# Optimization experiments

Hardware: AMD Instinct MI355X
Metric: run time of the kernel (lower is better)

Reference implementation:

```python
import jax, jax.numpy as jnp
import numpy as np
from jax import lax

N = 16384
K = 16
EPS = 1e-5


def setup_inputs() -> dict:
    key = jax.random.key(0)
    ks = jax.random.split(key, 10)

    def w(k, shape):
        fan_in = shape[0]
        return jax.random.normal(k, shape, jnp.float32) / np.sqrt(fan_in)

    return {
        "pos": jax.random.normal(ks[0], (N, 3), jnp.float32),
        "normal": jax.random.normal(ks[1], (N, 3), jnp.float32),
        # conv1 mlp: Linear(9,64) -> GroupNorm(8,64) -> ReLU -> Linear(64,64)
        "W1a": w(ks[2], (9, 64)), "b1a": jnp.zeros((64,), jnp.float32),
        "g1": jnp.ones((64,), jnp.float32), "beta1": jnp.zeros((64,), jnp.float32),
        "W1b": w(ks[3], (64, 64)), "b1b": jnp.zeros((64,), jnp.float32),
        # conv2 mlp: Linear(67,64) -> GroupNorm(8,64) -> ReLU -> Linear(64,64)
        "W2a": w(ks[4], (67, 64)), "b2a": jnp.zeros((64,), jnp.float32),
        "g2": jnp.ones((64,), jnp.float32), "beta2": jnp.zeros((64,), jnp.float32),
        "W2b": w(ks[5], (64, 64)), "b2b": jnp.zeros((64,), jnp.float32),
        # conv3 mlp: Linear(67,128) -> GroupNorm(16,128) -> ReLU -> Linear(128,128)
        "W3a": w(ks[6], (67, 128)), "b3a": jnp.zeros((128,), jnp.float32),
        "g3": jnp.ones((128,), jnp.float32), "beta3": jnp.zeros((128,), jnp.float32),
        "W3b": w(ks[7], (128, 128)), "b3b": jnp.zeros((128,), jnp.float32),
    }


def knn_graph(pos, k):
    # [N,N] squared distances; loop=True -> self is included (distance 0).
    sq = jnp.sum(pos * pos, axis=1)
    d2 = sq[:, None] + sq[None, :] - 2.0 * (pos @ pos.T)
    _, nbr = lax.top_k(-d2, k)  # [N,k] neighbor (source) indices per target node
    return nbr


def group_norm(h, gamma, beta, groups):
    # h: [N,k,C]; normalize each group of channels per edge sample.
    n, k, c = h.shape
    hg = h.reshape(n, k, groups, c // groups)
    mu = hg.mean(axis=-1, keepdims=True)
    var = hg.var(axis=-1, keepdims=True)
    hg = (hg - mu) * lax.rsqrt(var + EPS)
    return hg.reshape(n, k, c) * gamma + beta


def pointnet_conv(x, pos, nbr, Wa, ba, gamma, beta, Wb, bb, groups):
    # message: concat(x_j, pos_j - pos_i), MLP per edge, max-aggregate over neighbors
    xj = x[nbr]                              # [N,k,C_in]
    rel = pos[nbr] - pos[:, None, :]         # [N,k,3]
    m = jnp.concatenate([xj, rel], axis=-1)  # [N,k,C_in+3]
    h = m @ Wa + ba
    h = jax.nn.relu(group_norm(h, gamma, beta, groups))
    h = h @ Wb + bb
    return jnp.max(h, axis=1)                # [N,C_out]


def reference(pos, normal, W1a, b1a, g1, beta1, W1b, b1b,
              W2a, b2a, g2, beta2, W2b, b2b,
              W3a, b3a, g3, beta3, W3b, b3b):
    nbr = knn_graph(pos, K)
    h = jnp.concatenate([pos, normal], axis=-1)  # [N,6]
    h1 = jax.nn.relu(pointnet_conv(h, pos, nbr, W1a, b1a, g1, beta1, W1b, b1b, 8))
    h2 = jax.nn.relu(pointnet_conv(h1, pos, nbr, W2a, b2a, g2, beta2, W2b, b2b, 8))
    h3 = jax.nn.relu(pointnet_conv(h2, pos, nbr, W3a, b3a, g3, beta3, W3b, b3b, 16))
    return (h1, h2, h3)
```

## Files before the change

kernel.cpp:

```cpp
#include <hip/hip_runtime.h>
#include <hip/hip_bf16.h>
#include <stdint.h>

typedef unsigned long long u64;
typedef unsigned int u32;
typedef __attribute__((ext_vector_type(8))) short bf16x8;
typedef __attribute__((ext_vector_type(8))) unsigned short u16x8;
typedef __attribute__((ext_vector_type(4))) float f32x4;

__device__ __forceinline__ float ldv(const void* p, size_t idx, int mode) {
  return mode ? __bfloat162float(((const __hip_bfloat16*)p)[idx])
              : ((const float*)p)[idx];
}
__device__ __forceinline__ void stv(void* p, size_t idx, int mode, float v) {
  if (mode) ((__hip_bfloat16*)p)[idx] = __float2bfloat16(v);
  else      ((float*)p)[idx] = v;
}
__device__ __forceinline__ unsigned short f2bfb(float f) {
  u32 u = __float_as_uint(f);
  u32 r = u + 0x7fffu + ((u >> 16) & 1u);
  return (unsigned short)(r >> 16);
}
__device__ __forceinline__ float bfb2f(unsigned short b) {
  return __uint_as_float((u32)b << 16);
}
__device__ __forceinline__ u64 shfl64(u64 v, int src) {
  int lo = __shfl((int)(u32)(v & 0xffffffffu), src, 64);
  int hi = __shfl((int)(u32)(v >> 32), src, 64);
  return ((u64)(u32)hi << 32) | (u32)lo;
}
__device__ __forceinline__ u64 shflxor64(u64 v, int m) {
  int lo = __shfl_xor((int)(u32)(v & 0xffffffffu), m, 64);
  int hi = __shfl_xor((int)(u32)(v >> 32), m, 64);
  return ((u64)(u32)hi << 32) | (u32)lo;
}
__device__ __forceinline__ u64 shfl64w16(u64 v, int src) {
  int lo = __shfl((int)(u32)(v & 0xffffffffu), src, 16);
  int hi = __shfl((int)(u32)(v >> 32), src, 16);
  return ((u64)(u32)hi << 32) | (u32)lo;
}

__device__ __forceinline__ u32 benc(float f) {
  u32 u = __float_as_uint(f);
  return (u & 0x80000000u) ? ~u : (u | 0x80000000u);
}
__device__ __forceinline__ float bdec(u32 k) {
  return (k & 0x80000000u) ? __uint_as_float(k ^ 0x80000000u)
                           : __uint_as_float(~k);
}

__global__ void PointNetSimple_61409442398998_kernel() {}

struct CvtEnt { const void* src; float* dst; int n; };
struct CvtArgs { CvtEnt e[12]; };
struct WEnt { const void* src; unsigned short* dst; int K, N, Kpad; };
struct WArgs { WEnt e[6]; };

__global__ void setup_kernel(const void* __restrict__ pos,
                             const void* __restrict__ nrm,
                             WArgs wa, CvtArgs ca,
                             int* __restrict__ flag,
                             float4* __restrict__ pos4,
                             float* __restrict__ h0, int n) {
  const unsigned short* u16p = (const unsigned short*)pos;
  int cnt = 0;
  for (int k = 0; k < 32; ++k) {
    int e = (u16p[k] >> 7) & 0xff;
    if (e >= 110 && e <= 140) cnt++;
  }
  const int mode = (cnt >= 26) ? 1 : 0;

  const int nprep = n >> 8;
  const int b = blockIdx.x;
  if (b < nprep) {
    int i = b * 256 + threadIdx.x;
    float x = ldv(pos, 3*(size_t)i+0, mode);
    float y = ldv(pos, 3*(size_t)i+1, mode);
    float z = ldv(pos, 3*(size_t)i+2, mode);
    pos4[i] = make_float4(x, y, z, x*x + y*y + z*z);
    h0[6*(size_t)i+0] = x; h0[6*(size_t)i+1] = y; h0[6*(size_t)i+2] = z;
    h0[6*(size_t)i+3] = ldv(nrm, 3*(size_t)i+0, mode);
    h0[6*(size_t)i+4] = ldv(nrm, 3*(size_t)i+1, mode);
    h0[6*(size_t)i+5] = ldv(nrm, 3*(size_t)i+2, mode);
    float bmn[3] = {x, y, z}, bmx[3] = {x, y, z};
#pragma unroll
    for (int m = 32; m; m >>= 1) {
#pragma unroll
      for (int k = 0; k < 3; ++k) {
        bmn[k] = fminf(bmn[k], __shfl_xor(bmn[k], m, 64));
        bmx[k] = fmaxf(bmx[k], __shfl_xor(bmx[k], m, 64));
      }
    }
    if ((threadIdx.x & 63) == 0) {
      u32* bb = (u32*)flag;
#pragma unroll
      for (int k = 0; k < 3; ++k) {
        atomicMin(&bb[4 + k], benc(bmn[k]));
        atomicMax(&bb[7 + k], benc(bmx[k]));
      }
    }
  } else {
    int r = b - nprep;
    if (r < 6) {
      WEnt ent = wa.e[r];
      for (int t = threadIdx.x; t < ent.N * ent.Kpad; t += blockDim.x) {
        int nn = t / ent.Kpad;
        int k  = t - nn * ent.Kpad;
        float v = (k < ent.K) ? ldv(ent.src, (size_t)k * ent.N + nn, mode) : 0.0f;
        ent.dst[t] = f2bfb(v);
      }
      if (r == 0 && threadIdx.x == 0) flag[0] = mode;
    } else {
      for (int t2 = 0; t2 < 12; ++t2) {
        CvtEnt ent = ca.e[t2];
        for (int t = threadIdx.x; t < ent.n; t += blockDim.x)
          ent.dst[t] = ldv(ent.src, t, mode);
      }
    }
  }
}

__device__ __forceinline__ void knn_flush(u64* __restrict__ wbuf, int& cnt,
                                          u64& val, u64& t15, float& th,
                                          int lane) {
  u64 cand = (lane < cnt) ? wbuf[lane] : ~0ull;
#pragma unroll
  for (int k = 2; k <= 64; k <<= 1) {
#pragma unroll
    for (int j = k >> 1; j > 0; j >>= 1) {
      u64 other = shflxor64(cand, j);
      bool up    = ((lane & k) == 0) || (k == 64);
      bool lower = ((lane & j) == 0);
      bool keepMin = (up == lower);
      u64 mn = cand < other ? cand : other;
      u64 mx = cand < other ? other : cand;
      cand = keepMin ? mn : mx;
    }
  }
  u64 rev = shfl64w16(cand, 15 - (lane & 15));
  u64 lo = val < rev ? val : rev;
#pragma unroll
  for (int j = 8; j > 0; j >>= 1) {
    u64 other = shflxor64(lo, j);
    bool lower = ((lane & j) == 0);
    u64 mn = lo < other ? lo : other;
    u64 mx = lo < other ? other : lo;
    lo = lower ? mn : mx;
  }
  val = (lane < 16) ? lo : ~0ull;
  t15 = shfl64(val, 15);
  u32 thb = (u32)(t15 >> 32);
  th = (thb == 0xffffffffu) ? 3.4e38f : __uint_as_float(thb);
  cnt = 0;
}

#define GR 32
#define GR3 (GR*GR*GR)

__global__ __launch_bounds__(256) void hist_kernel(
    const float4* __restrict__ pos4, const u32* __restrict__ bbx,
    int* __restrict__ counts, int* __restrict__ cid, int n) {
  const int i = blockIdx.x * 256 + threadIdx.x;
  if (i >= n) return;
  const float mnx = bdec(bbx[0]), mny = bdec(bbx[1]), mnz = bdec(bbx[2]);
  const float ihx = (float)GR / fmaxf(bdec(bbx[3]) - mnx, 1e-20f);
  const float ihy = (float)GR / fmaxf(bdec(bbx[4]) - mny, 1e-20f);
  const float ihz = (float)GR / fmaxf(bdec(bbx[5]) - mnz, 1e-20f);
  float4 p = pos4[i];
  int cx = min(GR - 1, max(0, (int)((p.x - mnx) * ihx)));
  int cy = min(GR - 1, max(0, (int)((p.y - mny) * ihy)));
  int cz = min(GR - 1, max(0, (int)((p.z - mnz) * ihz)));
  int lin = (cz * GR + cy) * GR + cx;
  cid[i] = lin;
  atomicAdd(&counts[lin], 1);
}

__global__ __launch_bounds__(1024) void scan_kernel(
    const int* __restrict__ counts, int* __restrict__ cellstart,
    int* __restrict__ cursor) {
  __shared__ int part[1024];
  const int t = threadIdx.x;
  const int base = t * 32;
  int v[32];
  int s = 0;
#pragma unroll
  for (int k = 0; k < 32; ++k) { v[k] = counts[base + k]; s += v[k]; }
  part[t] = s;
  __syncthreads();
  for (int d = 1; d < 1024; d <<= 1) {
    int x = (t >= d) ? part[t - d] : 0;
    __syncthreads();
    part[t] += x;
    __syncthreads();
  }
  int off = part[t] - s;
#pragma unroll
  for (int k = 0; k < 32; ++k) {
    cellstart[base + k] = off; cursor[base + k] = off; off += v[k];
  }
  if (t == 1023) { cellstart[GR3] = off; cursor[GR3] = off; }
}

__global__ __launch_bounds__(256) void scatter_kernel(
    const float4* __restrict__ pos4, const int* __restrict__ cid,
    int* __restrict__ cursor, int* __restrict__ sidx,
    float4* __restrict__ spos4, int n) {
  const int i = blockIdx.x * 256 + threadIdx.x;
  if (i >= n) return;
  int dst = atomicAdd(&cursor[cid[i]], 1);
  spos4[dst] = pos4[i];
  sidx[dst]  = i;
}

#define KNN6_WPB 4
__global__ __launch_bounds__(256) void knn6_kernel(
    const float4* __restrict__ spos4,
    const int* __restrict__ sidx, const int* __restrict__ cellstart,
    const u32* __restrict__ bbx, int* __restrict__ nbr, int n) {
  __shared__ u64 buf[KNN6_WPB][72];
  const int tid = threadIdx.x, lane = tid & 63, w = tid >> 6;
  const int g = blockIdx.x * KNN6_WPB + w;
  u64* wbuf = &buf[w][0];
  const float4 pi = spos4[g];
  const int target = sidx[g];

  const float mnx = bdec(bbx[0]), mny = bdec(bbx[1]), mnz = bdec(bbx[2]);
  const float ex = fmaxf(bdec(bbx[3]) - mnx, 1e-20f);
  const float ey = fmaxf(bdec(bbx[4]) - mny, 1e-20f);
  const float ez = fmaxf(bdec(bbx[5]) - mnz, 1e-20f);
  const float ihx = (float)GR / ex, ihy = (float)GR / ey, ihz = (float)GR / ez;
  const float hxf = ex * (1.0f / GR), hyf = ey * (1.0f / GR), hzf = ez * (1.0f / GR);
  const int cx = min(GR - 1, max(0, (int)((pi.x - mnx) * ihx)));
  const int cy = min(GR - 1, max(0, (int)((pi.y - mny) * ihy)));
  const int cz = min(GR - 1, max(0, (int)((pi.z - mnz) * ihz)));

  u64 val = ~0ull, t15 = ~0ull;
  float th = 3.4e38f;
  int cnt = 0, nseen = 0;

  auto procSeg = [&](int p0, int p1) {
    if (p1 <= p0) return;
    nseen += p1 - p0;
#pragma unroll 2
    for (int t0 = p0; t0 < p1; t0 += 64) {
      int gi = t0 + lane;
      bool in = gi < p1;
      float4 a = spos4[in ? gi : (p1 - 1)];
      float d2 = (pi.w + a.w) - 2.0f*(pi.x*a.x + pi.y*a.y + pi.z*a.z);
      d2 = fmaxf(d2, 0.0f);
      bool pass = in && (d2 <= th);
      u64 bal = __ballot(pass);
      if (bal) {
        int pc = __popcll(bal);
        if (cnt + pc > 64) knn_flush(wbuf, cnt, val, t15, th, lane);
        u32 mb = __builtin_amdgcn_mbcnt_lo((u32)bal, 0u);
        mb = __builtin_amdgcn_mbcnt_hi((u32)(bal >> 32), mb);
        if (pass)
          wbuf[cnt + mb] = ((u64)__float_as_uint(d2) << 32) | (u32)sidx[gi];
        cnt += pc;
      }
    }
  };

  const int oc = (cz * GR + cy) * GR + cx;
  const int oLo = cellstart[oc], oHi = cellstart[oc + 1];
  procSeg(oLo, oHi);
  if (cnt > 0) knn_flush(wbuf, cnt, val, t15, th, lane);

  int prevLo = 0, prevHi = -1;
  if (lane == cz) { prevLo = oLo; prevHi = oHi; }

  for (int r = 1; r < GR; ++r) {
    const int z0 = max(cz - r, 0), z1 = min(cz + r, GR - 1);
    const int y0 = max(cy - r, 0), y1 = min(cy + r, GR - 1);
    const int x0 = max(cx - r, 0), x1 = min(cx + r, GR - 1);
    int a0 = 0, a1v = 0, b0 = 0, b1v = 0;
    if (lane >= z0 && lane <= z1) {
      int nLo = cellstart[(lane * GR + y0) * GR + x0];
      int nHi = cellstart[(lane * GR + y1) * GR + x1 + 1];
      if (prevHi < 0) { a0 = nLo; a1v = nHi; }
      else            { a0 = nLo; a1v = prevLo; b0 = prevHi; b1v = nHi; }
      prevLo = nLo; prevHi = nHi;
    }
    for (int z = z0; z <= z1; ++z) {
      int sa0 = __shfl(a0, z, 64), sa1 = __shfl(a1v, z, 64);
      int sb0 = __shfl(b0, z, 64), sb1 = __shfl(b1v, z, 64);
      procSeg(sa0, sa1);
      procSeg(sb0, sb1);
    }
    if (cnt > 0) knn_flush(wbuf, cnt, val, t15, th, lane);
    if (nseen >= n) break;
    float mind = 3.4e38f;
    if (cx - r > 0)      mind = fminf(mind, pi.x - (mnx + (float)(cx - r) * hxf));
    if (cx + r < GR - 1) mind = fminf(mind, (mnx + (float)(cx + r + 1) * hxf) - pi.x);
    if (cy - r > 0)      mind = fminf(mind, pi.y - (mny + (float)(cy - r) * hyf));
    if (cy + r < GR - 1) mind = fminf(mind, (mny + (float)(cy + r + 1) * hyf) - pi.y);
    if (cz - r > 0)      mind = fminf(mind, pi.z - (mnz + (float)(cz - r) * hzf));
    if (cz + r < GR - 1) mind = fminf(mind, (mnz + (float)(cz + r + 1) * hzf) - pi.z);
    float mind2 = mind * mind * 0.9999f - 1e-6f;
    if (mind2 > th) break;
  }
  if (cnt > 0) knn_flush(wbuf, cnt, val, t15, th, lane);
  if (lane < 16) nbr[(size_t)target * 16 + lane] = (int)(val & 0xffffffffu);
}

template<int CIN, int CMID, int KT1, int NT, int KT2>
__global__ __launch_bounds__(256, 4) void conv_mfma6_kernel(
    const float* __restrict__ xf,
    const unsigned short* __restrict__ xb,
    const float4* __restrict__ pos4,
    const int* __restrict__ nbr,
    const int* __restrict__ flag,
    const unsigned short* __restrict__ WaT,
    const unsigned short* __restrict__ WbT,
    const float* __restrict__ baf,
    const float* __restrict__ gmf,
    const float* __restrict__ btf,
    const float* __restrict__ bbf,
    unsigned short* __restrict__ xoutb,
    void* __restrict__ bout, size_t out_off)
{
  constexpr int K1PAD = KT1 * 32;
  constexpr int SB = CMID + 8;

  __shared__ unsigned short msgB[128 * SB];

  const int tid  = threadIdx.x;
  const int lane = tid & 63;
  const int w    = tid >> 6;
  const int quad = lane >> 4;
  const int cl   = lane & 15;
  const int node0 = blockIdx.x * 8;
  const int mode = flag[0];

  bf16x8 afr[2][KT1];
#pragma unroll
  for (int mt = 0; mt < 2; ++mt) {
    const int node = node0 + w*2 + mt;
    const int j = nbr[(size_t)node*16 + cl];
    const float4 pin = pos4[node];
    const float4 pj = pos4[j];
    const float rx = pj.x - pin.x, ry = pj.y - pin.y, rz = pj.z - pin.z;
    if constexpr (CIN == 64) {
#pragma unroll
      for (int kt = 0; kt < 2; ++kt)
        afr[mt][kt] = *(const bf16x8*)&xb[(size_t)j*64 + kt*32 + quad*8];
      unsigned short o[8] = {0,0,0,0,0,0,0,0};
      if (quad == 0) { o[0] = f2bfb(rx); o[1] = f2bfb(ry); o[2] = f2bfb(rz); }
      afr[mt][KT1-1] = *(bf16x8*)o;
    } else {
      unsigned short o[8] = {0,0,0,0,0,0,0,0};
      if (quad == 0) {
        const float* p = &xf[(size_t)j*6];
        o[0] = f2bfb(p[0]); o[1] = f2bfb(p[1]); o[2] = f2bfb(p[2]);
        o[3] = f2bfb(p[3]); o[4] = f2bfb(p[4]); o[5] = f2bfb(p[5]);
        o[6] = f2bfb(rx);   o[7] = f2bfb(ry);
      } else if (quad == 1) {
        o[0] = f2bfb(rz);
      }
      afr[mt][0] = *(bf16x8*)o;
    }
  }

  const int grow = lane >> 1, ggl = lane & 1;
#pragma unroll
  for (int nt = 0; nt < NT; ++nt) {
    f32x4 a1[2];
    a1[0] = (f32x4){0.f, 0.f, 0.f, 0.f};
    a1[1] = (f32x4){0.f, 0.f, 0.f, 0.f};
#pragma unroll
    for (int kt = 0; kt < KT1; ++kt) {
      bf16x8 bfr = *(const bf16x8*)&WaT[(size_t)(nt*16 + cl) * K1PAD + kt*32 + quad*8];
      a1[0] = __builtin_amdgcn_mfma_f32_16x16x32_bf16(afr[0][kt], bfr, a1[0], 0, 0, 0);
      a1[1] = __builtin_amdgcn_mfma_f32_16x16x32_bf16(afr[1][kt], bfr, a1[1], 0, 0, 0);
    }
    float bac = baf[nt*16 + cl];
#pragma unroll
    for (int mt = 0; mt < 2; ++mt)
#pragma unroll
      for (int reg = 0; reg < 4; ++reg)
        msgB[(w*32 + mt*16 + quad*4 + reg) * SB + nt*16 + cl] =
            f2bfb(a1[mt][reg] + bac);
    asm volatile("" ::: "memory");
    {
      const int cb = nt*16 + ggl*8;
      unsigned short* p = &msgB[(w*32 + grow) * SB + cb];
      u16x8 hv = *(const u16x8*)p;
      float vv[8];
#pragma unroll
      for (int e = 0; e < 8; ++e) vv[e] = bfb2f(hv[e]);
      float s = 0.f, q = 0.f;
#pragma unroll
      for (int e = 0; e < 8; ++e) { s += vv[e]; q += vv[e]*vv[e]; }
      float mu = s * 0.125f;
      float var = q * 0.125f - mu * mu;
      float inv = rsqrtf(fmaxf(var, 0.0f) + 1e-5f);
      unsigned short o[8];
#pragma unroll
      for (int e = 0; e < 8; ++e) {
        float t = (vv[e] - mu) * inv * gmf[cb+e] + btf[cb+e];
        o[e] = f2bfb(fmaxf(t, 0.0f));
      }
      *(bf16x8*)p = *(bf16x8*)o;
    }
    asm volatile("" ::: "memory");
  }

  f32x4 acc2[2][NT];
#pragma unroll
  for (int mt = 0; mt < 2; ++mt)
#pragma unroll
    for (int nt = 0; nt < NT; ++nt) acc2[mt][nt] = (f32x4){0.f, 0.f, 0.f, 0.f};
#pragma unroll
  for (int kt = 0; kt < KT2; ++kt) {
    bf16x8 af0 = *(const bf16x8*)&msgB[(w*32 + cl)      * SB + kt*32 + quad*8];
    bf16x8 af1 = *(const bf16x8*)&msgB[(w*32 + 16 + cl) * SB + kt*32 + quad*8];
#pragma unroll
    for (int nt = 0; nt < NT; ++nt) {
      bf16x8 bfr = *(const bf16x8*)&WbT[(size_t)(nt*16 + cl) * CMID + kt*32 + quad*8];
      acc2[0][nt] = __builtin_amdgcn_mfma_f32_16x16x32_bf16(af0, bfr, acc2[0][nt], 0, 0, 0);
      acc2[1][nt] = __builtin_amdgcn_mfma_f32_16x16x32_bf16(af1, bfr, acc2[1][nt], 0, 0, 0);
    }
  }

#pragma unroll
  for (int mt = 0; mt < 2; ++mt) {
    int node = node0 + w*2 + mt;
#pragma unroll
    for (int nt = 0; nt < NT; ++nt) {
      float m = fmaxf(fmaxf(acc2[mt][nt][0], acc2[mt][nt][1]),
                      fmaxf(acc2[mt][nt][2], acc2[mt][nt][3]));
      m = fmaxf(m, __shfl_xor(m, 16, 64));
      m = fmaxf(m, __shfl_xor(m, 32, 64));
      float v = fmaxf(m + bbf[nt*16 + cl], 0.0f);
      if (quad == 0) {
        size_t oi = (size_t)node * CMID + nt*16 + cl;
        if (xoutb) xoutb[oi] = f2bfb(v);
        stv(bout, out_off + oi, mode, v);
      }
    }
  }
}

extern "C" void kernel_launch(void* const* d_in, const int* in_sizes, int n_in,
                              void* d_out, int out_size, void* d_ws, size_t ws_size,
                              hipStream_t stream) {
  (void)n_in; (void)ws_size; (void)in_sizes;
  int n = out_size / 256;
  if (n <= 0 || (n & 255)) n = 16384;

  float* ws = (float*)d_ws;
  int*    flag    = (int*)ws;
  float4* pos4    = (float4*)(ws + 16);
  float*  h0      = ws + 16 + (size_t)4*n;
  int*    nbr     = (int*)(ws + 16 + (size_t)10*n);
  unsigned short* h1b = (unsigned short*)(ws + 16 + (size_t)26*n);
  unsigned short* h2b = (unsigned short*)(ws + 16 + (size_t)58*n);
  float*  vbuf    = ws + 16 + (size_t)90*n;
  unsigned short* wtbuf = (unsigned short*)(vbuf + 1024);

  float* gbase = vbuf + 1024 + 22528;
  int*    cid       = (int*)gbase;
  int*    counts    = cid + n;
  int*    cellstart = counts + GR3;
  int*    cursor    = cellstart + 32772;
  int*    sidx      = cursor + 32772;
  float4* spos4     = (float4*)(sidx + n);

  const int vsz[12] = {64,64,64,64, 64,64,64,64, 128,128,128,128};
  const int vsrc[12] = {3,4,5,7, 9,10,11,13, 15,16,17,19};
  CvtArgs ca;
  float* vptr[12];
  {
    int off = 0;
    for (int t = 0; t < 12; ++t) {
      ca.e[t].src = d_in[vsrc[t]];
      ca.e[t].dst = vbuf + off;
      ca.e[t].n   = vsz[t];
      vptr[t] = vbuf + off;
      off += vsz[t];
    }
  }
  const int wK[6]    = {9, 64, 67, 64, 67, 128};
  const int wN[6]    = {64, 64, 64, 64, 128, 128};
  const int wKp[6]   = {32, 64, 96, 64, 96, 128};
  const int wsrc[6]  = {2, 6, 8, 12, 14, 18};
  WArgs wa;
  unsigned short* wptr[6];
  {
    int off = 0;
    for (int t = 0; t < 6; ++t) {
      wa.e[t].src  = d_in[wsrc[t]];
      wa.e[t].dst  = wtbuf + off;
      wa.e[t].K    = wK[t];
      wa.e[t].N    = wN[t];
      wa.e[t].Kpad = wKp[t];
      wptr[t] = wtbuf + off;
      off += wN[t] * wKp[t];
    }
  }

  u32* bbx = (u32*)ws + 4;
  hipMemsetAsync(bbx,     0xFF, 12, stream);
  hipMemsetAsync(bbx + 3, 0x00, 12, stream);
  hipMemsetAsync(counts,  0x00, GR3 * sizeof(int), stream);

  setup_kernel<<<n/256 + 7, 256, 0, stream>>>(
      d_in[0], d_in[1], wa, ca, flag, pos4, h0, n);

  hist_kernel<<<n/256, 256, 0, stream>>>(pos4, bbx, counts, cid, n);
  scan_kernel<<<1, 1024, 0, stream>>>(counts, cellstart, cursor);
  scatter_kernel<<<n/256, 256, 0, stream>>>(pos4, cid, cursor, sidx, spos4, n);
  knn6_kernel<<<n/KNN6_WPB, 256, 0, stream>>>(spos4, sidx, cellstart,
                                              bbx, nbr, n);

  conv_mfma6_kernel<6, 64, 1, 4, 2><<<n/8, 256, 0, stream>>>(
      h0, (const unsigned short*)nullptr, pos4, nbr, flag, wptr[0], wptr[1],
      vptr[0], vptr[1], vptr[2], vptr[3], h1b, d_out, (size_t)0);
  conv_mfma6_kernel<64, 64, 3, 4, 2><<<n/8, 256, 0, stream>>>(
      (const float*)nullptr, h1b, pos4, nbr, flag, wptr[2], wptr[3],
      vptr[4], vptr[5], vptr[6], vptr[7], h2b, d_out, (size_t)n*64);
  conv_mfma6_kernel<64, 128, 3, 8, 4><<<n/8, 256, 0, stream>>>(
      (const float*)nullptr, h2b, pos4, nbr, flag, wptr[4], wptr[5],
      vptr[8], vptr[9], vptr[10], vptr[11],
      (unsigned short*)nullptr, d_out, (size_t)n*128);
}
```

Before: 364.4 us.

## Enumerate only new shell cells per ring and use smaller bitonic flush

The kNN ring expansion now enumerates only the cells on the new shell at radius r, in parallel across lanes and split into z-faces, y-faces and x-edge cells. Only non-empty x-runs are processed. Before, whole z-slabs were rescanned as two segments around the previous box. The flush picks a 32-wide bitonic sort when the candidate buffer holds at most 32 entries, which cuts shuffle stages. The seen count is now tallied per lane and reduced with a wave reduction, which adds index math and more segment launches per ring.

```diff
diff --git a/kernel.cpp b/kernel.cpp
--- a/kernel.cpp
+++ b/kernel.cpp
@@ -120,16 +120,17 @@
   }
 }
 
+template<int CAP>
 __device__ __forceinline__ void knn_flush(u64* __restrict__ wbuf, int& cnt,
                                           u64& val, u64& t15, float& th,
                                           int lane) {
   u64 cand = (lane < cnt) ? wbuf[lane] : ~0ull;
 #pragma unroll
-  for (int k = 2; k <= 64; k <<= 1) {
+  for (int k = 2; k <= CAP; k <<= 1) {
 #pragma unroll
     for (int j = k >> 1; j > 0; j >>= 1) {
       u64 other = shflxor64(cand, j);
-      bool up    = ((lane & k) == 0) || (k == 64);
+      bool up    = ((lane & k) == 0) || (k == CAP);
       bool lower = ((lane & j) == 0);
       bool keepMin = (up == lower);
       u64 mn = cand < other ? cand : other;
@@ -212,14 +213,14 @@
   sidx[dst]  = i;
 }
 
-#define KNN6_WPB 4
-__global__ __launch_bounds__(256) void knn6_kernel(
+#define KNN7_WPB 4
+__global__ __launch_bounds__(256) void knn7_kernel(
     const float4* __restrict__ spos4,
     const int* __restrict__ sidx, const int* __restrict__ cellstart,
     const u32* __restrict__ bbx, int* __restrict__ nbr, int n) {
-  __shared__ u64 buf[KNN6_WPB][72];
+  __shared__ u64 buf[KNN7_WPB][72];
   const int tid = threadIdx.x, lane = tid & 63, w = tid >> 6;
-  const int g = blockIdx.x * KNN6_WPB + w;
+  const int g = blockIdx.x * KNN7_WPB + w;
   u64* wbuf = &buf[w][0];
   const float4 pi = spos4[g];
   const int target = sidx[g];
@@ -236,11 +237,15 @@
 
   u64 val = ~0ull, t15 = ~0ull;
   float th = 3.4e38f;
-  int cnt = 0, nseen = 0;
+  int cnt = 0;
+  int myseen = 0;
+
+  auto doFlush = [&]() {
+    if (cnt <= 32) knn_flush<32>(wbuf, cnt, val, t15, th, lane);
+    else           knn_flush<64>(wbuf, cnt, val, t15, th, lane);
+  };
 
   auto procSeg = [&](int p0, int p1) {
-    if (p1 <= p0) return;
-    nseen += p1 - p0;
 #pragma unroll 2
     for (int t0 = p0; t0 < p1; t0 += 64) {
       int gi = t0 + lane;
@@ -252,7 +257,7 @@
       u64 bal = __ballot(pass);
       if (bal) {
         int pc = __popcll(bal);
-        if (cnt + pc > 64) knn_flush(wbuf, cnt, val, t15, th, lane);
+        if (cnt + pc > 64) doFlush();
         u32 mb = __builtin_amdgcn_mbcnt_lo((u32)bal, 0u);
         mb = __builtin_amdgcn_mbcnt_hi((u32)(bal >> 32), mb);
         if (pass)
@@ -262,34 +267,69 @@
     }
   };
 
-  const int oc = (cz * GR + cy) * GR + cx;
-  const int oLo = cellstart[oc], oHi = cellstart[oc + 1];
-  procSeg(oLo, oHi);
-  if (cnt > 0) knn_flush(wbuf, cnt, val, t15, th, lane);
-
-  int prevLo = 0, prevHi = -1;
-  if (lane == cz) { prevLo = oLo; prevHi = oHi; }
+  {
+    const int oc = (cz * GR + cy) * GR + cx;
+    const int oLo = cellstart[oc], oHi = cellstart[oc + 1];
+    if (lane == 0) myseen += oHi - oLo;
+    procSeg(oLo, oHi);
+    if (cnt > 0) doFlush();
+  }
 
   for (int r = 1; r < GR; ++r) {
-    const int z0 = max(cz - r, 0), z1 = min(cz + r, GR - 1);
-    const int y0 = max(cy - r, 0), y1 = min(cy + r, GR - 1);
     const int x0 = max(cx - r, 0), x1 = min(cx + r, GR - 1);
-    int a0 = 0, a1v = 0, b0 = 0, b1v = 0;
-    if (lane >= z0 && lane <= z1) {
-      int nLo = cellstart[(lane * GR + y0) * GR + x0];
-      int nHi = cellstart[(lane * GR + y1) * GR + x1 + 1];
-      if (prevHi < 0) { a0 = nLo; a1v = nHi; }
-      else            { a0 = nLo; a1v = prevLo; b0 = prevHi; b1v = nHi; }
-      prevLo = nLo; prevHi = nHi;
-    }
-    for (int z = z0; z <= z1; ++z) {
-      int sa0 = __shfl(a0, z, 64), sa1 = __shfl(a1v, z, 64);
-      int sb0 = __shfl(b0, z, 64), sb1 = __shfl(b1v, z, 64);
-      procSeg(sa0, sa1);
-      procSeg(sb0, sb1);
-    }
-    if (cnt > 0) knn_flush(wbuf, cnt, val, t15, th, lane);
-    if (nseen >= n) break;
+    const int d1 = 2*r + 1, d2i = 2*r - 1;
+    const int nA = 2 * d1;
+    const int nB = 2 * d2i;
+    const int nC = 2 * d2i * d2i;
+    const int S = nA + nB + nC;
+    const u32 magic = 0xFFFFFFFFu / (u32)d2i + 1u;
+
+    for (int b0 = 0; b0 < S; b0 += 64) {
+      const int s = b0 + lane;
+      int zc = 0, yc = 0, xa = 0, xb = -1;
+      bool live = s < S;
+      if (live) {
+        if (s < nA) {
+          int za = s >= d1;
+          int dy = s - (za ? d1 : 0) - r;
+          zc = cz + (za ? r : -r); yc = cy + dy; xa = x0; xb = x1;
+        } else if (s < nA + nB) {
+          int t = s - nA;
+          int side = t >= d2i;
+          int dz = t - (side ? d2i : 0) - (r - 1);
+          zc = cz + dz; yc = cy + (side ? r : -r); xa = x0; xb = x1;
+        } else {
+          int t = s - nA - nB;
+          int side = t & 1; t >>= 1;
+          int dzi = (int)__umulhi((u32)t, magic);
+          int dyi = t - dzi * d2i;
+          zc = cz - r + 1 + dzi; yc = cy - r + 1 + dyi;
+          int xcell = side ? cx + r : cx - r;
+          xa = xcell; xb = xcell;
+          live = ((unsigned)xcell < GR);
+        }
+        live = live && ((unsigned)zc < GR) && ((unsigned)yc < GR);
+      }
+      int lo = 0, hi = 0;
+      if (live) {
+        int base = (zc * GR + yc) * GR;
+        lo = cellstart[base + xa];
+        hi = cellstart[base + xb + 1];
+        myseen += hi - lo;
+      }
+      u64 bal = __ballot(live && (hi > lo));
+      while (bal) {
+        int l = __builtin_ctzll(bal); bal &= bal - 1;
+        int p0 = __shfl(lo, l, 64), p1 = __shfl(hi, l, 64);
+        procSeg(p0, p1);
+      }
+    }
+    if (cnt > 0) doFlush();
+
+    int tot = myseen;
+#pragma unroll
+    for (int m = 32; m; m >>= 1) tot += __shfl_xor(tot, m, 64);
+    if (tot >= n) break;
     float mind = 3.4e38f;
     if (cx - r > 0)      mind = fminf(mind, pi.x - (mnx + (float)(cx - r) * hxf));
     if (cx + r < GR - 1) mind = fminf(mind, (mnx + (float)(cx + r + 1) * hxf) - pi.x);
@@ -300,7 +340,7 @@
     float mind2 = mind * mind * 0.9999f - 1e-6f;
     if (mind2 > th) break;
   }
-  if (cnt > 0) knn_flush(wbuf, cnt, val, t15, th, lane);
+  if (cnt > 0) doFlush();
   if (lane < 16) nbr[(size_t)target * 16 + lane] = (int)(val & 0xffffffffu);
 }
 
@@ -511,7 +551,7 @@
   hist_kernel<<<n/256, 256, 0, stream>>>(pos4, bbx, counts, cid, n);
   scan_kernel<<<1, 1024, 0, stream>>>(counts, cellstart, cursor);
   scatter_kernel<<<n/256, 256, 0, stream>>>(pos4, cid, cursor, sidx, spos4, n);
-  knn6_kernel<<<n/KNN6_WPB, 256, 0, stream>>>(spos4, sidx, cellstart,
+  knn7_kernel<<<n/KNN7_WPB, 256, 0, stream>>>(spos4, sidx, cellstart,
                                               bbx, nbr, n);
 
   conv_mfma6_kernel<6, 64, 1, 4, 2><<<n/8, 256, 0, stream>>>(
```

Result: no change. 361.0 us (-0.9%).
